# Kernel optimization log

Measured on AMD Instinct MI355X. Metric: run time of the kernel, lower is better.

The kernel has to match this reference:

```python
import jax, jax.numpy as jnp
import numpy as np

# Forest of B perfect binary trees, depth D levels, M = 2**D - 1 nodes/tree.
B, D, H, X, VOCAB, NCLS = 32, 12, 256, 256, 32000, 20
M = 2 ** D - 1          # 4095 nodes per tree
N = B * M               # 131040 total nodes


def setup_inputs() -> dict:
    key = jax.random.key(0)
    ks = jax.random.split(key, 9)
    x = jax.random.randint(ks[0], (N,), 0, VOCAB, dtype=jnp.int32)
    # leaves are the last level of each tree: in-tree index >= 2**(D-1)-1
    leaf = (jnp.arange(M) >= 2 ** (D - 1) - 1).astype(jnp.int32)
    x_mask = jnp.tile(leaf, B)  # [N] int32, 1 on leaves, 0 on internal nodes
    s = 0.02
    Emb = jax.random.normal(ks[1], (VOCAB, X), jnp.float32) * s
    W_iou = jax.random.normal(ks[2], (3 * H, X), jnp.float32) * s
    b_iou = jnp.zeros((3 * H,), jnp.float32)
    U_iou = jax.random.normal(ks[3], (3 * H, H), jnp.float32) * s
    U_f = jax.random.normal(ks[4], (H, H), jnp.float32) * s
    b_f = jnp.ones((H,), jnp.float32)  # forget-gate bias init
    W_out = jax.random.normal(ks[5], (NCLS, H), jnp.float32) * s
    b_out = jnp.zeros((NCLS,), jnp.float32)
    return {"x": x, "x_mask": x_mask, "Emb": Emb, "W_iou": W_iou,
            "b_iou": b_iou, "U_iou": U_iou, "U_f": U_f, "b_f": b_f,
            "W_out": W_out, "b_out": b_out}


def reference(x, x_mask, Emb, W_iou, b_iou, U_iou, U_f, b_f, W_out, b_out):
    # input_module: embedding applied to masked ids, result masked again
    x_emb = Emb[x * x_mask] * x_mask[:, None].astype(Emb.dtype)      # [N, X]
    xiou = (x_emb @ W_iou.T).reshape(B, M, 3 * H)                    # W_iou * x per node
    h_sum = jnp.zeros((B, M, H), Emb.dtype)    # sum of children h (childsum)
    fc_sum = jnp.zeros((B, M, H), Emb.dtype)   # sum_k f_k * c_k from children
    h_all = jnp.zeros((B, M, H), Emb.dtype)
    # topological propagation: leaves (deepest level) -> roots
    for l in range(D - 1, -1, -1):
        s_, e_ = 2 ** l - 1, 2 ** (l + 1) - 1  # static in-tree level slice
        iou = xiou[:, s_:e_] + h_sum[:, s_:e_] @ U_iou.T + b_iou
        i, o, u = jnp.split(iou, 3, axis=-1)
        c = jax.nn.sigmoid(i) * jnp.tanh(u) + fc_sum[:, s_:e_]
        h = jax.nn.sigmoid(o) * jnp.tanh(c)
        h_all = h_all.at[:, s_:e_].set(h)
        if l > 0:
            f = jax.nn.sigmoid(h @ U_f.T + b_f)          # per-child forget gate
            parents = (np.arange(s_, e_) - 1) // 2       # static parent indices
            h_sum = h_sum.at[:, parents].add(h)
            fc_sum = fc_sum.at[:, parents].add(f * c)
    # output_module applied to all node states
    return h_all.reshape(N, H) @ W_out.T + b_out                    # [N, NCLS]
```

## Files before the change

kernel.cpp:

```cpp
#include <hip/hip_runtime.h>

#define B_TREES 32
#define DEPTH   12
#define M_NODES 4095
#define N_NODES (B_TREES * M_NODES)
#define HDIM    256
#define VOCAB   32000
#define NCLS    20
#define LEAFROWS 65536
#define LDSH_S 20

typedef _Float16 f16;
typedef _Float16 f16x8 __attribute__((ext_vector_type(8)));
typedef _Float16 f16x4 __attribute__((ext_vector_type(4)));
typedef _Float16 f16x2 __attribute__((ext_vector_type(2)));
typedef float    f32x4 __attribute__((ext_vector_type(4)));

__device__ __forceinline__ float sigf(float x)      { return 1.0f / (1.0f + __expf(-x)); }
__device__ __forceinline__ float tanh_fast(float x) { return 1.0f - 2.0f / (1.0f + __expf(2.0f * x)); }

__global__ __launch_bounds__(256) void cvt_kernel(
    const float4* __restrict__ Emb,  const float4* __restrict__ Wiou,
    const float4* __restrict__ Uiou, const float4* __restrict__ Uf,
    const float4* __restrict__ Wout,
    f16x4* __restrict__ Emb16,  f16x4* __restrict__ Wiou16,
    f16x4* __restrict__ Uiou16, f16x4* __restrict__ Uf16,
    f16x4* __restrict__ Wout16)
{
    int i = blockIdx.x * 256 + threadIdx.x;
    if (i < VOCAB * HDIM / 4) {
        float4 v = Emb[i];
        f16x4 r; r[0] = (f16)v.x; r[1] = (f16)v.y; r[2] = (f16)v.z; r[3] = (f16)v.w;
        Emb16[i] = r;
    }
    if (i < 768 * HDIM / 4) {
        float4 v = Wiou[i];
        f16x4 r; r[0] = (f16)v.x; r[1] = (f16)v.y; r[2] = (f16)v.z; r[3] = (f16)v.w;
        Wiou16[i] = r;
        float4 u = Uiou[i];
        f16x4 s; s[0] = (f16)u.x; s[1] = (f16)u.y; s[2] = (f16)u.z; s[3] = (f16)u.w;
        Uiou16[i] = s;
    }
    if (i < HDIM * HDIM / 4) {
        float4 v = Uf[i];
        f16x4 r; r[0] = (f16)v.x; r[1] = (f16)v.y; r[2] = (f16)v.z; r[3] = (f16)v.w;
        Uf16[i] = r;
    }
    if (i < 32 * HDIM / 4) {
        int row = i >> 6;
        f16x4 r = {};
        if (row < NCLS) {
            float4 v = Wout[i];
            r[0] = (f16)v.x; r[1] = (f16)v.y; r[2] = (f16)v.z; r[3] = (f16)v.w;
        }
        Wout16[i] = r;
    }
}

#define VTPW 5
__global__ __launch_bounds__(256) void vocab_kernel(
    const f16* __restrict__ Emb16, const f16* __restrict__ Wiou16,
    const float* __restrict__ b_iou,
    f16* __restrict__ hv, f16* __restrict__ cv)
{
    __shared__ f16 wlds[1536 * 8];
    __shared__ f16 ldshH[4][16 * LDSH_S];
    __shared__ f16 ldshC[4][16 * LDSH_S];

    const int tid  = threadIdx.x;
    const int lane = tid & 63;
    const int w    = tid >> 6;
    const int quad = lane >> 4;
    const int l15  = lane & 15;
    const int qk   = quad * 8;
    const int cb0  = blockIdx.y * 16;

    #pragma unroll
    for (int i = 0; i < 6; ++i) {
        int f = i * 256 + tid;
        int mat = f >> 9, r = f & 511, ks = r >> 6, q = (r >> 4) & 3, c = r & 15;
        *(f16x8*)(wlds + f * 8) = *(const f16x8*)(Wiou16 +
            (mat * 256 + cb0 + c) * HDIM + ks * 32 + q * 8);
    }
    __syncthreads();

    const float bi = b_iou[cb0 + l15];
    const float bo = b_iou[256 + cb0 + l15];
    const float bu = b_iou[512 + cb0 + l15];

    const int row0 = (blockIdx.x * 4 + w) * (VTPW * 16);

    f16x8 a[8];
    #pragma unroll
    for (int ks = 0; ks < 8; ++ks)
        a[ks] = *(const f16x8*)(Emb16 + (row0 + l15) * HDIM + ks * 32 + qk);

    for (int rt = 0; rt < VTPW; ++rt) {
        const int rw = row0 + rt * 16;
        f16x8 ac[8];
        #pragma unroll
        for (int ks = 0; ks < 8; ++ks) ac[ks] = a[ks];

        if (rt + 1 < VTPW) {
            #pragma unroll
            for (int ks = 0; ks < 8; ++ks)
                a[ks] = *(const f16x8*)(Emb16 + (rw + 16 + l15) * HDIM + ks * 32 + qk);
        }

        f32x4 acc[3] = {};
        #pragma unroll
        for (int ks = 0; ks < 8; ++ks) {
            #pragma unroll
            for (int mat = 0; mat < 3; ++mat) {
                f16x8 wf = *(const f16x8*)(wlds +
                    ((mat * 8 + ks) * 64 + quad * 16 + l15) * 8);
                acc[mat] = __builtin_amdgcn_mfma_f32_16x16x32_f16(
                    ac[ks], wf, acc[mat], 0, 0, 0);
            }
        }

        #pragma unroll
        for (int r = 0; r < 4; ++r) {
            float i_ = acc[0][r] + bi;
            float o_ = acc[1][r] + bo;
            float u_ = acc[2][r] + bu;
            float c  = sigf(i_) * tanh_fast(u_);
            float h  = sigf(o_) * tanh_fast(c);
            ldshH[w][(quad * 4 + r) * LDSH_S + l15] = (f16)h;
            ldshC[w][(quad * 4 + r) * LDSH_S + l15] = (f16)c;
        }

        {
            int row_l = lane >> 2, cpos = (lane & 3) * 4;
            f16x4 vh = *(const f16x4*)(&ldshH[w][row_l * LDSH_S + cpos]);
            *(f16x4*)(hv + (rw + row_l) * HDIM + cb0 + cpos) = vh;
            f16x4 vc = *(const f16x4*)(&ldshC[w][row_l * LDSH_S + cpos]);
            *(f16x4*)(cv + (rw + row_l) * HDIM + cb0 + cpos) = vc;
        }
    }
}

__global__ __launch_bounds__(256) void vocab_out_kernel(
    const f16* __restrict__ hv, const f16* __restrict__ Wout16,
    const float* __restrict__ bout, float* __restrict__ out_v)
{
    const int lane = threadIdx.x & 63;
    const int w    = threadIdx.x >> 6;
    const int quad = lane >> 4;
    const int l15  = lane & 15;
    const int qk   = quad * 8;

    f16x8 wfk[2][8];
    #pragma unroll
    for (int cf = 0; cf < 2; ++cf)
        #pragma unroll
        for (int ks = 0; ks < 8; ++ks)
            wfk[cf][ks] = *(const f16x8*)(Wout16 +
                (cf * 16 + l15) * HDIM + ks * 32 + qk);
    float bo[2];
    #pragma unroll
    for (int cf = 0; cf < 2; ++cf) {
        int col = cf * 16 + l15;
        bo[cf] = bout[col < NCLS ? col : 0];
    }

    const int tile0 = blockIdx.x * 16;

    for (int rt = w; rt < 16; rt += 4) {
        const int rw = (tile0 + rt) * 16;
        f32x4 acc[2] = {};
        #pragma unroll
        for (int ks = 0; ks < 8; ++ks) {
            f16x8 a = *(const f16x8*)(hv + (rw + l15) * HDIM + ks * 32 + qk);
            #pragma unroll
            for (int cf = 0; cf < 2; ++cf)
                acc[cf] = __builtin_amdgcn_mfma_f32_16x16x32_f16(
                    a, wfk[cf][ks], acc[cf], 0, 0, 0);
        }
        #pragma unroll
        for (int cf = 0; cf < 2; ++cf) {
            const int col = cf * 16 + l15;
            if (col < NCLS) {
                #pragma unroll
                for (int r = 0; r < 4; ++r)
                    out_v[(rw + quad * 4 + r) * NCLS + col] = acc[cf][r] + bo[cf];
            }
        }
    }
}

__global__ __launch_bounds__(256) void leaf_scatter_kernel(
    const int* __restrict__ x, const f16* __restrict__ hv,
    const f16* __restrict__ cv, const float* __restrict__ out_v,
    f16* __restrict__ h16, f16* __restrict__ cT, float* __restrict__ out)
{
    __shared__ int ids[64];
    __shared__ f16 ldsc[64][HDIM + 8];

    const int tid = threadIdx.x;
    const int R0  = blockIdx.x * 64;

    if (tid < 64) {
        int r = R0 + tid;
        int node = (r >> 11) * M_NODES + 2047 + (r & 2047);
        ids[tid] = x[node];
    }
    __syncthreads();

    const int r    = tid >> 2;
    const int p    = tid & 3;
    const int id   = ids[r];
    const int gr   = R0 + r;
    const int node = (gr >> 11) * M_NODES + 2047 + (gr & 2047);

    #pragma unroll
    for (int j = 0; j < 8; ++j) {
        f16x8 v = *(const f16x8*)(hv + id * HDIM + p * 64 + j * 8);
        *(f16x8*)(h16 + node * HDIM + p * 64 + j * 8) = v;
    }
    #pragma unroll
    for (int j = 0; j < 8; ++j) {
        f16x8 v = *(const f16x8*)(cv + id * HDIM + p * 64 + j * 8);
        *(f16x8*)(&ldsc[r][p * 64 + j * 8]) = v;
    }
    #pragma unroll
    for (int j = 0; j < 5; ++j)
        out[node * NCLS + p * 5 + j] = out_v[id * NCLS + p * 5 + j];

    __syncthreads();

    {
        const int c = tid;
        f16 tmp[64];
        #pragma unroll
        for (int rr = 0; rr < 64; ++rr) tmp[rr] = ldsc[rr][c];
        #pragma unroll
        for (int j = 0; j < 8; ++j)
            *(f16x8*)(cT + c * LEAFROWS + R0 + j * 8) = *(const f16x8*)(&tmp[j * 8]);
    }
}

__global__ __launch_bounds__(256) void fused_level_kernel(
    const f16* __restrict__ Uiou16, const f16* __restrict__ Uf16,
    const float* __restrict__ b_iou, const float* __restrict__ b_f,
    f16* __restrict__ h16, const f16* __restrict__ cT_child,
    f16* __restrict__ cT_parent, int l, int rows_p, int tpw)
{
    __shared__ f16 wlds[2048 * 8];
    __shared__ f16 ldsh[4][16 * LDSH_S];

    const int tid  = threadIdx.x;
    const int lane = tid & 63;
    const int w    = tid >> 6;
    const int quad = lane >> 4;
    const int l15  = lane & 15;
    const int qk   = quad * 8;
    const int cb0  = blockIdx.y * 16;

    #pragma unroll
    for (int i = 0; i < 8; ++i) {
        int f = i * 256 + tid;
        int mat = f >> 9, r = f & 511, ks = r >> 6, q = (r >> 4) & 3, c = r & 15;
        const f16* src = (mat == 0)
            ? (Uf16 + (cb0 + c) * HDIM + ks * 32 + q * 8)
            : (Uiou16 + ((mat - 1) * 256 + cb0 + c) * HDIM + ks * 32 + q * 8);
        *(f16x8*)(wlds + f * 8) = *(const f16x8*)src;
    }
    __syncthreads();

    const float bi  = b_iou[cb0 + l15];
    const float bo  = b_iou[256 + cb0 + l15];
    const float bu  = b_iou[512 + cb0 + l15];
    const float bfv = b_f[cb0 + l15];
    const int lc = l + 1;
    const int maskc = (1 << lc) - 1;
    const int maskp = (1 << l) - 1;
    const int rows_c = rows_p * 2;

    const int p0 = blockIdx.x * (tpw * 64);

    for (int pt = 0; pt < tpw; ++pt) {
        const int pw = p0 + (pt * 4 + w) * 16;
        if (pw >= rows_p) continue;
        const int cw = 2 * pw;

        int childBase0, childBase1;
        {
            int cl0 = cw + l15;
            childBase0 = ((cl0 >> lc) * M_NODES + maskc + (cl0 & maskc)) * HDIM;
            int cl1 = cw + 16 + l15;
            childBase1 = ((cl1 >> lc) * M_NODES + maskc + (cl1 & maskc)) * HDIM;
        }

        f32x4 accf0 = {}, accf1 = {};
        f32x4 au0[3] = {}, au1[3] = {};
        #pragma unroll
        for (int ks = 0; ks < 8; ++ks) {
            const int k0 = ks * 32 + qk;
            f16x8 a0 = *(const f16x8*)(h16 + childBase0 + k0);
            f16x8 a1 = *(const f16x8*)(h16 + childBase1 + k0);
            f16x8 wfF = *(const f16x8*)(wlds + (ks * 64 + quad * 16 + l15) * 8);
            accf0 = __builtin_amdgcn_mfma_f32_16x16x32_f16(a0, wfF, accf0, 0, 0, 0);
            accf1 = __builtin_amdgcn_mfma_f32_16x16x32_f16(a1, wfF, accf1, 0, 0, 0);
            #pragma unroll
            for (int m = 0; m < 3; ++m) {
                f16x8 wm = *(const f16x8*)(wlds +
                    (((m + 1) * 8 + ks) * 64 + quad * 16 + l15) * 8);
                au0[m] = __builtin_amdgcn_mfma_f32_16x16x32_f16(a0, wm, au0[m], 0, 0, 0);
                au1[m] = __builtin_amdgcn_mfma_f32_16x16x32_f16(a1, wm, au1[m], 0, 0, 0);
            }
        }

        #pragma unroll
        for (int s = 0; s < 2; ++s) {
            const f32x4& af = s ? accf1 : accf0;
            const f32x4* au = s ? au1 : au0;
            const int csr = cw + s * 16;
            f16x4 cc = *(const f16x4*)(cT_child +
                (cb0 + l15) * rows_c + csr + quad * 4);
            f16x2 cpack;
            #pragma unroll
            for (int pr = 0; pr < 2; ++pr) {
                float f0 = sigf(af[2 * pr]     + bfv);
                float f1 = sigf(af[2 * pr + 1] + bfv);
                float fc = f0 * (float)cc[2 * pr] + f1 * (float)cc[2 * pr + 1];
                float i_ = au[0][2 * pr] + au[0][2 * pr + 1] + bi;
                float o_ = au[1][2 * pr] + au[1][2 * pr + 1] + bo;
                float u_ = au[2][2 * pr] + au[2][2 * pr + 1] + bu;
                float c  = sigf(i_) * tanh_fast(u_) + fc;
                float h  = sigf(o_) * tanh_fast(c);
                cpack[pr] = (f16)c;
                ldsh[w][(s * 8 + quad * 2 + pr) * LDSH_S + l15] = (f16)h;
            }
            *(f16x2*)(cT_parent + (cb0 + l15) * rows_p + pw + s * 8 + quad * 2) = cpack;
        }

        {
            int prow = lane >> 2, cpos = (lane & 3) * 4;
            int p = pw + prow;
            int b = p >> l, tt = p & maskp;
            int node = b * M_NODES + (1 << l) - 1 + tt;
            f16x4 v = *(const f16x4*)(&ldsh[w][prow * LDSH_S + cpos]);
            *(f16x4*)(h16 + node * HDIM + cb0 + cpos) = v;
        }
    }
}

__global__ __launch_bounds__(256) void out_kernel(
    const f16* __restrict__ h16, const f16* __restrict__ Wout16,
    const float* __restrict__ bout, float* __restrict__ out)
{
    const int lane = threadIdx.x & 63;
    const int w    = threadIdx.x >> 6;
    const int quad = lane >> 4;
    const int l15  = lane & 15;
    const int qk   = quad * 8;

    f16x8 wfk[2][8];
    #pragma unroll
    for (int cf = 0; cf < 2; ++cf)
        #pragma unroll
        for (int ks = 0; ks < 8; ++ks)
            wfk[cf][ks] = *(const f16x8*)(Wout16 +
                (cf * 16 + l15) * HDIM + ks * 32 + qk);
    float bo[2];
    #pragma unroll
    for (int cf = 0; cf < 2; ++cf) {
        int col = cf * 16 + l15;
        bo[cf] = bout[col < NCLS ? col : 0];
    }

    const int tile0 = blockIdx.x * 16;

    for (int rt = w; rt < 16; rt += 4) {
        const int tt = tile0 + rt;
        const int rw = (tt >> 7) * M_NODES + (tt & 127) * 16;
        f32x4 acc[2] = {};
        #pragma unroll
        for (int ks = 0; ks < 8; ++ks) {
            f16x8 a = *(const f16x8*)(h16 + (rw + l15) * HDIM + ks * 32 + qk);
            #pragma unroll
            for (int cf = 0; cf < 2; ++cf)
                acc[cf] = __builtin_amdgcn_mfma_f32_16x16x32_f16(
                    a, wfk[cf][ks], acc[cf], 0, 0, 0);
        }
        #pragma unroll
        for (int cf = 0; cf < 2; ++cf) {
            const int col = cf * 16 + l15;
            if (col < NCLS) {
                #pragma unroll
                for (int r = 0; r < 4; ++r)
                    out[(rw + quad * 4 + r) * NCLS + col] = acc[cf][r] + bo[cf];
            }
        }
    }
}

extern "C" void kernel_launch(void* const* d_in, const int* in_sizes, int n_in,
                              void* d_out, int out_size, void* d_ws, size_t ws_size,
                              hipStream_t stream)
{
    const int*   x     = (const int*)d_in[0];
    const float* Emb   = (const float*)d_in[2];
    const float* W_iou = (const float*)d_in[3];
    const float* b_iou = (const float*)d_in[4];
    const float* U_iou = (const float*)d_in[5];
    const float* U_f   = (const float*)d_in[6];
    const float* b_f   = (const float*)d_in[7];
    const float* W_out = (const float*)d_in[8];
    const float* b_out = (const float*)d_in[9];
    float* out = (float*)d_out;

    char* ws = (char*)d_ws;
    size_t off = 0;
    auto take = [&](size_t bytes) -> char* {
        char* p = ws + off; off += (bytes + 255) & ~(size_t)255; return p;
    };
    f16* h16    = (f16*)take((size_t)N_NODES * HDIM * 2);
    f16* cA     = (f16*)take((size_t)HDIM * LEAFROWS * 2);
    f16* cB     = (f16*)take((size_t)HDIM * (LEAFROWS / 2) * 2);
    f16* Emb16  = (f16*)take((size_t)VOCAB * HDIM * 2);
    f16* Wiou16 = (f16*)take((size_t)768 * HDIM * 2);
    f16* Uiou16 = (f16*)take((size_t)768 * HDIM * 2);
    f16* Uf16   = (f16*)take((size_t)HDIM * HDIM * 2);
    f16* Wout16 = (f16*)take((size_t)32 * HDIM * 2);
    f16* cv     = (f16*)take((size_t)VOCAB * HDIM * 2);
    float* outv = (float*)take((size_t)VOCAB * NCLS * 4);
    f16* hv     = cB;

    cvt_kernel<<<VOCAB * HDIM / 4 / 256, 256, 0, stream>>>(
        (const float4*)Emb, (const float4*)W_iou, (const float4*)U_iou,
        (const float4*)U_f, (const float4*)W_out,
        (f16x4*)Emb16, (f16x4*)Wiou16, (f16x4*)Uiou16, (f16x4*)Uf16,
        (f16x4*)Wout16);

    vocab_kernel<<<dim3(VOCAB / (4 * 16 * VTPW), 16), 256, 0, stream>>>(
        Emb16, Wiou16, b_iou, hv, cv);

    vocab_out_kernel<<<dim3(VOCAB / 16 / 16), 256, 0, stream>>>(
        hv, Wout16, b_out, outv);

    leaf_scatter_kernel<<<dim3(LEAFROWS / 64), 256, 0, stream>>>(
        x, hv, cv, outv, h16, cA, out);

    f16* cin  = cA;
    f16* cout_ = cB;
    for (int l = 10; l >= 0; --l) {
        int rows_p = B_TREES << l;
        int tpw = rows_p / (64 * 128); if (tpw < 1) tpw = 1;
        int gx  = (rows_p + tpw * 64 - 1) / (tpw * 64);
        fused_level_kernel<<<dim3(gx, 16), 256, 0, stream>>>(
            Uiou16, Uf16, b_iou, b_f, h16, cin, cout_, l, rows_p, tpw);
        f16* t = cin; cin = cout_; cout_ = t;
    }

    out_kernel<<<dim3(32 * 128 / 16), 256, 0, stream>>>(
        h16, Wout16, b_out, out);
}
```

Measured before the change: 410.1 us.

## Sum sibling hidden states before the iou MFMA and prefetch next tile's child rows

Each wave now handles 16 parents, holding even and odd children in separate operands. The two child h vectors are added in f16 before the U_iou multiply, so the three iou MFMAs run once per parent instead of once per child. The forget-gate MFMAs still run per child. The next tile's child h rows are prefetched into registers while the current tile computes, and the tiles-per-wave choice per level is changed. The f16 sibling sum adds a little rounding error and the double-buffered registers raise register pressure.

Result: slower. 425.4 us (+3.7%).

```diff
diff --git a/kernel.cpp b/kernel.cpp
--- a/kernel.cpp
+++ b/kernel.cpp
@@ -279,61 +279,75 @@
 
     const int p0 = blockIdx.x * (tpw * 64);
 
+    auto cbase = [&](int cl) {
+        return ((cl >> lc) * M_NODES + maskc + (cl & maskc)) * HDIM;
+    };
+
+    f16x8 ae[8], ao[8];
+    {
+        int pw0 = p0 + w * 16;
+        if (pw0 < rows_p) {
+            int be = cbase(2 * pw0 + 2 * l15);
+            int bd = cbase(2 * pw0 + 2 * l15 + 1);
+            #pragma unroll
+            for (int ks = 0; ks < 8; ++ks) {
+                ae[ks] = *(const f16x8*)(h16 + be + ks * 32 + qk);
+                ao[ks] = *(const f16x8*)(h16 + bd + ks * 32 + qk);
+            }
+        }
+    }
+
     for (int pt = 0; pt < tpw; ++pt) {
         const int pw = p0 + (pt * 4 + w) * 16;
         if (pw >= rows_p) continue;
-        const int cw = 2 * pw;
-
-        int childBase0, childBase1;
-        {
-            int cl0 = cw + l15;
-            childBase0 = ((cl0 >> lc) * M_NODES + maskc + (cl0 & maskc)) * HDIM;
-            int cl1 = cw + 16 + l15;
-            childBase1 = ((cl1 >> lc) * M_NODES + maskc + (cl1 & maskc)) * HDIM;
-        }
-
-        f32x4 accf0 = {}, accf1 = {};
-        f32x4 au0[3] = {}, au1[3] = {};
+
+        f16x8 ce[8], co[8];
+        #pragma unroll
+        for (int ks = 0; ks < 8; ++ks) { ce[ks] = ae[ks]; co[ks] = ao[ks]; }
+
+        if (pt + 1 < tpw) {
+            int be = cbase(2 * (pw + 64) + 2 * l15);
+            int bd = cbase(2 * (pw + 64) + 2 * l15 + 1);
+            #pragma unroll
+            for (int ks = 0; ks < 8; ++ks) {
+                ae[ks] = *(const f16x8*)(h16 + be + ks * 32 + qk);
+                ao[ks] = *(const f16x8*)(h16 + bd + ks * 32 + qk);
+            }
+        }
+
+        f32x4 accfe = {}, accfo = {};
+        f32x4 aiou[3] = {};
         #pragma unroll
         for (int ks = 0; ks < 8; ++ks) {
-            const int k0 = ks * 32 + qk;
-            f16x8 a0 = *(const f16x8*)(h16 + childBase0 + k0);
-            f16x8 a1 = *(const f16x8*)(h16 + childBase1 + k0);
+            f16x8 hs  = ce[ks] + co[ks];
             f16x8 wfF = *(const f16x8*)(wlds + (ks * 64 + quad * 16 + l15) * 8);
-            accf0 = __builtin_amdgcn_mfma_f32_16x16x32_f16(a0, wfF, accf0, 0, 0, 0);
-            accf1 = __builtin_amdgcn_mfma_f32_16x16x32_f16(a1, wfF, accf1, 0, 0, 0);
+            accfe = __builtin_amdgcn_mfma_f32_16x16x32_f16(ce[ks], wfF, accfe, 0, 0, 0);
+            accfo = __builtin_amdgcn_mfma_f32_16x16x32_f16(co[ks], wfF, accfo, 0, 0, 0);
             #pragma unroll
             for (int m = 0; m < 3; ++m) {
                 f16x8 wm = *(const f16x8*)(wlds +
                     (((m + 1) * 8 + ks) * 64 + quad * 16 + l15) * 8);
-                au0[m] = __builtin_amdgcn_mfma_f32_16x16x32_f16(a0, wm, au0[m], 0, 0, 0);
-                au1[m] = __builtin_amdgcn_mfma_f32_16x16x32_f16(a1, wm, au1[m], 0, 0, 0);
-            }
-        }
-
-        #pragma unroll
-        for (int s = 0; s < 2; ++s) {
-            const f32x4& af = s ? accf1 : accf0;
-            const f32x4* au = s ? au1 : au0;
-            const int csr = cw + s * 16;
-            f16x4 cc = *(const f16x4*)(cT_child +
-                (cb0 + l15) * rows_c + csr + quad * 4);
-            f16x2 cpack;
-            #pragma unroll
-            for (int pr = 0; pr < 2; ++pr) {
-                float f0 = sigf(af[2 * pr]     + bfv);
-                float f1 = sigf(af[2 * pr + 1] + bfv);
-                float fc = f0 * (float)cc[2 * pr] + f1 * (float)cc[2 * pr + 1];
-                float i_ = au[0][2 * pr] + au[0][2 * pr + 1] + bi;
-                float o_ = au[1][2 * pr] + au[1][2 * pr + 1] + bo;
-                float u_ = au[2][2 * pr] + au[2][2 * pr + 1] + bu;
-                float c  = sigf(i_) * tanh_fast(u_) + fc;
-                float h  = sigf(o_) * tanh_fast(c);
-                cpack[pr] = (f16)c;
-                ldsh[w][(s * 8 + quad * 2 + pr) * LDSH_S + l15] = (f16)h;
-            }
-            *(f16x2*)(cT_parent + (cb0 + l15) * rows_p + pw + s * 8 + quad * 2) = cpack;
-        }
+                aiou[m] = __builtin_amdgcn_mfma_f32_16x16x32_f16(hs, wm, aiou[m], 0, 0, 0);
+            }
+        }
+
+        f16x8 cc = *(const f16x8*)(cT_child +
+            (cb0 + l15) * rows_c + 2 * pw + quad * 8);
+        f16x4 cpk;
+        #pragma unroll
+        for (int r = 0; r < 4; ++r) {
+            float f0 = sigf(accfe[r] + bfv);
+            float f1 = sigf(accfo[r] + bfv);
+            float fc = f0 * (float)cc[2 * r] + f1 * (float)cc[2 * r + 1];
+            float i_ = aiou[0][r] + bi;
+            float o_ = aiou[1][r] + bo;
+            float u_ = aiou[2][r] + bu;
+            float c  = sigf(i_) * tanh_fast(u_) + fc;
+            float h  = sigf(o_) * tanh_fast(c);
+            cpk[r] = (f16)c;
+            ldsh[w][(quad * 4 + r) * LDSH_S + l15] = (f16)h;
+        }
+        *(f16x4*)(cT_parent + (cb0 + l15) * rows_p + pw + quad * 4) = cpk;
 
         {
             int prow = lane >> 2, cpos = (lane & 3) * 4;
@@ -447,7 +461,7 @@
     f16* cout_ = cB;
     for (int l = 10; l >= 0; --l) {
         int rows_p = B_TREES << l;
-        int tpw = rows_p / (64 * 128); if (tpw < 1) tpw = 1;
+        int tpw = (rows_p >= 32768) ? 4 : (rows_p >= 8192 ? 2 : 1);
         int gx  = (rows_p + tpw * 64 - 1) / (tpw * 64);
         fused_level_kernel<<<dim3(gx, 16), 256, 0, stream>>>(
             Uiou16, Uf16, b_iou, b_f, h16, cin, cout_, l, rows_p, tpw);
```
